# Performance work log

Measured on AMD Instinct MI355X. Metric: run time of the kernel, lower is better.

## Reference

```python
import jax, jax.numpy as jnp
import numpy as np

N_NODES = 50000
N_EDGES = 800000
D_IN = 128
D_OUT = 128
NEG_SLOPE = 0.2


def setup_inputs() -> dict:
    key = jax.random.key(0)
    ks = jax.random.split(key, 6)
    stdv = 1.0 / np.sqrt(D_OUT)
    X = jax.random.normal(ks[0], (N_NODES, D_IN), dtype=jnp.float32)
    W = jax.random.uniform(ks[1], (D_IN, D_OUT), dtype=jnp.float32, minval=-stdv, maxval=stdv)
    W_r = jax.random.uniform(ks[2], (D_IN, D_OUT), dtype=jnp.float32, minval=-stdv, maxval=stdv)
    W_l = jax.random.uniform(ks[3], (D_IN, D_OUT), dtype=jnp.float32, minval=-stdv, maxval=stdv)
    src = jax.random.randint(ks[4], (N_EDGES,), 0, N_NODES, dtype=jnp.int32)
    dst = jax.random.randint(ks[5], (N_EDGES,), 0, N_NODES, dtype=jnp.int32)
    return {"X": X, "W": W, "W_r": W_r, "W_l": W_l, "src": src, "dst": dst}


def reference(X, W, W_r, W_l, src, dst):
    # Dense transforms (comb/agg feature paths)
    comb = X @ W            # [N, D_out]
    h_r = X @ W_r           # [N, D_out]
    h_l = X @ W_l           # [N, D_out]
    # SDDMM: per-edge score e_ij = dot(h_l[i], h_r[j]) at nonzeros of A
    e = jnp.sum(h_l[src] * h_r[dst], axis=-1)          # [E]
    e = jax.nn.leaky_relu(e, negative_slope=NEG_SLOPE)  # LeakyReLU(0.2) on edge values
    # SpMM aggregation: agg[i] = sum_{j in N(i)} e_ij * comb[j]
    msgs = e[:, None] * comb[dst]                       # [E, D_out]
    agg = jax.ops.segment_sum(msgs, src, num_segments=N_NODES)  # [N, D_out]
    return agg
```

## Files before the change

### kernel.cpp

```cpp
#include <hip/hip_runtime.h>
#include <hip/hip_bf16.h>

#define N_NODES 50000
#define N_EDGES 800000
#define D 128
#define NEG_SLOPE 0.2f
#define APAD 136

#define FB 196
#define BCAP 8192
#define CHUNK 4096
#define BIN_NBLK ((N_EDGES + CHUNK - 1) / CHUNK)
#define CONV_NBLK (N_NODES * D / 4 / 256)
#define GEMM_LDS ((D + 64) * APAD * 2)

typedef __attribute__((ext_vector_type(8))) short bf16x8;
typedef __attribute__((ext_vector_type(4))) float f32x4;

__device__ inline unsigned short f2bf(float f) {
    union { float f; unsigned u; } v; v.f = f;
    const unsigned r = v.u + 0x7FFF + ((v.u >> 16) & 1);
    return (unsigned short)(r >> 16);
}
__device__ inline unsigned fbits(float f) { union { float f; unsigned u; } v; v.f = f; return v.u; }
__device__ inline float ffrom(unsigned u) { union { unsigned u; float f; } v; v.u = u; return v.f; }

__device__ inline void unpack8(const float4 raw, float* o) {
    const unsigned w0 = fbits(raw.x), w1 = fbits(raw.y), w2 = fbits(raw.z), w3 = fbits(raw.w);
    o[0] = ffrom(w0 << 16); o[1] = ffrom(w0 & 0xffff0000u);
    o[2] = ffrom(w1 << 16); o[3] = ffrom(w1 & 0xffff0000u);
    o[4] = ffrom(w2 << 16); o[5] = ffrom(w2 & 0xffff0000u);
    o[6] = ffrom(w3 << 16); o[7] = ffrom(w3 & 0xffff0000u);
}

__device__ inline int scan256_incl(int* arr, int t, int v) {
    arr[t] = v; __syncthreads();
#pragma unroll
    for (int off = 1; off < 256; off <<= 1) {
        const int u = (t >= off) ? arr[t - off] : 0;
        __syncthreads();
        arr[t] += u;
        __syncthreads();
    }
    return arr[t];
}

__global__ __launch_bounds__(256) void convert_prep_kernel(const float4* __restrict__ X,
                                                           ushort4* __restrict__ Xb,
                                                           const float* __restrict__ W_l,
                                                           const float* __restrict__ W_r,
                                                           const float* __restrict__ W,
                                                           ushort* __restrict__ MbT,
                                                           ushort* __restrict__ WbT,
                                                           int* __restrict__ bucket_fill) {
    if (blockIdx.x < CONV_NBLK) {
        const int i = blockIdx.x * 256 + threadIdx.x;
        const float4 v = X[i];
        ushort4 o;
        o.x = f2bf(v.x); o.y = f2bf(v.y); o.z = f2bf(v.z); o.w = f2bf(v.w);
        Xb[i] = o;
    } else {
        if (blockIdx.x == CONV_NBLK) bucket_fill[threadIdx.x] = 0;
        const int a = (blockIdx.x - CONV_NBLK) * 2 + (threadIdx.x >> 7);
        const int b2 = threadIdx.x & 127;
        float acc = 0.f;
#pragma unroll
        for (int c = 0; c < D; c += 4) {
            const float4 wl = *(const float4*)(W_l + a * D + c);
            const float4 wr = *(const float4*)(W_r + b2 * D + c);
            acc += wl.x * wr.x + wl.y * wr.y + wl.z * wr.z + wl.w * wr.w;
        }
        MbT[b2 * D + a] = f2bf(acc);
        WbT[b2 * D + a] = f2bf(W[a * D + b2]);
    }
}

__global__ __launch_bounds__(256) void bin_kernel(const int* __restrict__ src,
                                                  const int* __restrict__ dst,
                                                  int* __restrict__ bucket_fill,
                                                  int2* __restrict__ binned) {
    __shared__ int hist[256];
    __shared__ int bstart[256];
    __shared__ int reserveS[256];
    __shared__ int fillL[256];
    __shared__ int2 pairs[CHUNK];
    __shared__ int targ[CHUNK];
    const int t = threadIdx.x;
    const int e0 = blockIdx.x * CHUNK;

    hist[t] = 0;
    __syncthreads();

    int s[16], d[16], b[16];
#pragma unroll
    for (int i = 0; i < 16; ++i) {
        const int e = e0 + i * 256 + t;
        if (e < N_EDGES) {
            s[i] = src[e]; d[i] = dst[e]; b[i] = s[i] >> 8;
            atomicAdd(&hist[b[i]], 1);
        } else b[i] = -1;
    }
    __syncthreads();
    const int hv = hist[t];
    const int incl = scan256_incl(bstart, t, hv);
    const int mystart = incl - hv;
    reserveS[t] = hv ? atomicAdd(&bucket_fill[t], hv) : 0;
    __syncthreads();
    bstart[t] = mystart;
    fillL[t] = mystart;
    __syncthreads();
#pragma unroll
    for (int i = 0; i < 16; ++i) {
        if (b[i] >= 0) {
            const int p = atomicAdd(&fillL[b[i]], 1);
            pairs[p] = make_int2(s[i], d[i]);
            const int pos = reserveS[b[i]] + (p - bstart[b[i]]);
            targ[p] = (pos < BCAP) ? (b[i] * BCAP + pos) : -1;
        }
    }
    __syncthreads();
    const int nval = min(CHUNK, N_EDGES - e0);
    for (int j = t; j < nval; j += 256)
        if (targ[j] >= 0) binned[targ[j]] = pairs[j];
}

template <bool OUT_F32>
__device__ __forceinline__ void gemm_body(char* smemraw, int blk,
                                          const ushort* __restrict__ A,
                                          const ushort* __restrict__ BT,
                                          float* __restrict__ Cf,
                                          ushort* __restrict__ Cb,
                                          int nrows) {
    unsigned short* Bs = (unsigned short*)smemraw;
    unsigned short* As = Bs + D * APAD;
    const int tid = threadIdx.x;
    const int rb = blk * 64;

#pragma unroll
    for (int i = 0; i < 8; ++i) {
        const int idx = tid + i * 256;
        const int row = idx >> 4;
        const int c8 = (idx & 15) << 3;
        const float4 v = ((const float4*)BT)[idx];
        *(float4*)&Bs[row * APAD + c8] = v;
    }
#pragma unroll
    for (int i = 0; i < 4; ++i) {
        const int idx = tid + i * 256;
        const int row = idx >> 4;
        const int c8 = (idx & 15) << 3;
        float4 v = {0.f, 0.f, 0.f, 0.f};
        if (rb + row < nrows)
            v = ((const float4*)(A + (size_t)(rb + row) * D))[idx & 15];
        *(float4*)&As[row * APAD + c8] = v;
    }
    __syncthreads();

    const int w = tid >> 6;
    const int lane = tid & 63;
    const int m = lane & 15;
    const int kq = lane >> 4;

    f32x4 acc[8] = {};
    const unsigned short* Arow = &As[(w * 16 + m) * APAD + kq * 8];
#pragma unroll
    for (int kc = 0; kc < 4; ++kc) {
        const bf16x8 af = *(const bf16x8*)(Arow + kc * 32);
#pragma unroll
        for (int t2 = 0; t2 < 8; ++t2) {
            const bf16x8 bf = *(const bf16x8*)&Bs[(t2 * 16 + m) * APAD + kc * 32 + kq * 8];
            acc[t2] = __builtin_amdgcn_mfma_f32_16x16x32_bf16(af, bf, acc[t2], 0, 0, 0);
        }
    }

    const int orow0 = rb + w * 16 + kq * 4;
#pragma unroll
    for (int t2 = 0; t2 < 8; ++t2) {
#pragma unroll
        for (int r = 0; r < 4; ++r) {
            const int row = orow0 + r;
            if (row < nrows) {
                const size_t o = (size_t)row * D + t2 * 16 + m;
                if (OUT_F32) Cf[o] = acc[t2][r];
                else         Cb[o] = f2bf(acc[t2][r]);
            }
        }
    }
}

__global__ __launch_bounds__(256) void fine_gemm1_kernel(const int2* __restrict__ binned,
                                                         const int* __restrict__ bucket_fill,
                                                         int* __restrict__ offsets,
                                                         int* __restrict__ sorted_dst,
                                                         const ushort* __restrict__ Xb,
                                                         const ushort* __restrict__ MbT,
                                                         ushort* __restrict__ hMb) {
    __shared__ __align__(16) char smem[GEMM_LDS];
    if (blockIdx.x >= FB) {
        gemm_body<false>(smem, blockIdx.x - FB, Xb, MbT, nullptr, hMb, N_NODES);
        return;
    }
    int* cntS   = (int*)smem;
    int* nh     = cntS + 256;
    int* ex     = nh + 256;
    int* fill   = ex + 256;
    int* dstbuf = fill + 256;

    const int b = blockIdx.x;
    const int t = threadIdx.x;

    const int myc = (t < FB) ? bucket_fill[t] : 0;
    scan256_incl(cntS, t, myc);
    const int base = (b == 0) ? 0 : cntS[b - 1];
    int cnt = cntS[b] - base;
    if (cnt > BCAP) cnt = BCAP;

    nh[t] = 0;
    __syncthreads();
    const int2* bb = binned + (size_t)b * BCAP;
    for (int e = t; e < cnt; e += 256) atomicAdd(&nh[bb[e].x & 255], 1);
    __syncthreads();
    const int v = nh[t];
    const int incl2 = scan256_incl(ex, t, v);
    const int mystart = incl2 - v;
    const int node = b * 256 + t;
    if (node < N_NODES) offsets[node] = base + mystart;
    fill[t] = mystart;
    __syncthreads();
    for (int e = t; e < cnt; e += 256) {
        const int2 sd = bb[e];
        const int p = atomicAdd(&fill[sd.x & 255], 1);
        dstbuf[p] = sd.y;
    }
    __syncthreads();
    for (int j = t; j < cnt; j += 256)
        sorted_dst[base + j] = dstbuf[j];
}

__global__ __launch_bounds__(256) void gemm2_kernel(const ushort* __restrict__ A,
                                                    const ushort* __restrict__ BT,
                                                    float* __restrict__ Cf) {
    __shared__ __align__(16) char smem[GEMM_LDS];
    gemm_body<true>(smem, blockIdx.x, A, BT, Cf, nullptr, N_NODES);
}

__global__ __launch_bounds__(256) void spmm_kernel(const ushort* __restrict__ hMb,
                                                   const ushort* __restrict__ Xb,
                                                   const int* __restrict__ offsets,
                                                   const int* __restrict__ sorted_dst,
                                                   ushort* __restrict__ aggXb) {
    const int wave = threadIdx.x >> 6;
    const int lane = threadIdx.x & 63;
    const int node = blockIdx.x * 4 + wave;
    const int q = lane >> 4;
    const int ql = lane & 15;

    float hm[8];
    unpack8(*(const float4*)(hMb + (size_t)node * D + ql * 8), hm);

    const int start = offsets[node];
    const int end = (node == N_NODES - 1) ? N_EDGES : offsets[node + 1];

    float acc[8] = {0.f, 0.f, 0.f, 0.f, 0.f, 0.f, 0.f, 0.f};

    int idx = start + q;
    while (idx + 12 < end) {
        const int d0 = sorted_dst[idx];
        const int d1 = sorted_dst[idx + 4];
        const int d2 = sorted_dst[idx + 8];
        const int d3 = sorted_dst[idx + 12];
        const float4 r0 = *(const float4*)(Xb + (size_t)d0 * D + ql * 8);
        const float4 r1 = *(const float4*)(Xb + (size_t)d1 * D + ql * 8);
        const float4 r2 = *(const float4*)(Xb + (size_t)d2 * D + ql * 8);
        const float4 r3 = *(const float4*)(Xb + (size_t)d3 * D + ql * 8);
        float t0 = 0.f, t1 = 0.f, t2 = 0.f, t3 = 0.f;
        {
            float x[8];
            unpack8(r0, x);
#pragma unroll
            for (int j = 0; j < 8; ++j) t0 = fmaf(hm[j], x[j], t0);
            unpack8(r1, x);
#pragma unroll
            for (int j = 0; j < 8; ++j) t1 = fmaf(hm[j], x[j], t1);
            unpack8(r2, x);
#pragma unroll
            for (int j = 0; j < 8; ++j) t2 = fmaf(hm[j], x[j], t2);
            unpack8(r3, x);
#pragma unroll
            for (int j = 0; j < 8; ++j) t3 = fmaf(hm[j], x[j], t3);
        }
#pragma unroll
        for (int mm = 1; mm < 16; mm <<= 1) {
            t0 += __shfl_xor(t0, mm);
            t1 += __shfl_xor(t1, mm);
            t2 += __shfl_xor(t2, mm);
            t3 += __shfl_xor(t3, mm);
        }
        const float e0 = t0 > 0.f ? t0 : NEG_SLOPE * t0;
        const float e1 = t1 > 0.f ? t1 : NEG_SLOPE * t1;
        const float e2 = t2 > 0.f ? t2 : NEG_SLOPE * t2;
        const float e3 = t3 > 0.f ? t3 : NEG_SLOPE * t3;
        {
            float x[8];
            unpack8(r0, x);
#pragma unroll
            for (int j = 0; j < 8; ++j) acc[j] = fmaf(e0, x[j], acc[j]);
            unpack8(r1, x);
#pragma unroll
            for (int j = 0; j < 8; ++j) acc[j] = fmaf(e1, x[j], acc[j]);
            unpack8(r2, x);
#pragma unroll
            for (int j = 0; j < 8; ++j) acc[j] = fmaf(e2, x[j], acc[j]);
            unpack8(r3, x);
#pragma unroll
            for (int j = 0; j < 8; ++j) acc[j] = fmaf(e3, x[j], acc[j]);
        }
        idx += 16;
    }
    while (idx < end) {
        const int d0 = sorted_dst[idx];
        const float4 r0 = *(const float4*)(Xb + (size_t)d0 * D + ql * 8);
        float x[8];
        unpack8(r0, x);
        float t0 = 0.f;
#pragma unroll
        for (int j = 0; j < 8; ++j) t0 = fmaf(hm[j], x[j], t0);
#pragma unroll
        for (int mm = 1; mm < 16; mm <<= 1) t0 += __shfl_xor(t0, mm);
        const float e0 = t0 > 0.f ? t0 : NEG_SLOPE * t0;
#pragma unroll
        for (int j = 0; j < 8; ++j) acc[j] = fmaf(e0, x[j], acc[j]);
        idx += 4;
    }

#pragma unroll
    for (int j = 0; j < 8; ++j) {
        acc[j] += __shfl_xor(acc[j], 16);
        acc[j] += __shfl_xor(acc[j], 32);
    }
    if (q == 0) {
        ushort4 o0, o1;
        o0.x = f2bf(acc[0]); o0.y = f2bf(acc[1]); o0.z = f2bf(acc[2]); o0.w = f2bf(acc[3]);
        o1.x = f2bf(acc[4]); o1.y = f2bf(acc[5]); o1.z = f2bf(acc[6]); o1.w = f2bf(acc[7]);
        ushort* outp = aggXb + (size_t)node * D + ql * 8;
        *(ushort4*)outp = o0;
        *(ushort4*)(outp + 4) = o1;
    }
}

extern "C" void kernel_launch(void* const* d_in, const int* in_sizes, int n_in,
                              void* d_out, int out_size, void* d_ws, size_t ws_size,
                              hipStream_t stream) {
    const float* X   = (const float*)d_in[0];
    const float* W   = (const float*)d_in[1];
    const float* W_r = (const float*)d_in[2];
    const float* W_l = (const float*)d_in[3];
    const int* src   = (const int*)d_in[4];
    const int* dst   = (const int*)d_in[5];
    float* agg = (float*)d_out;

    ushort* Xb          = (ushort*)d_ws;
    ushort* hMb         = Xb + (size_t)N_NODES * D;
    ushort* aggXb       = hMb + (size_t)N_NODES * D;
    ushort* MbT         = aggXb + (size_t)N_NODES * D;
    ushort* WbT         = MbT + D * D;
    int*    offsets     = (int*)(WbT + D * D);
    int*    sorted_dst  = offsets + N_NODES;
    int*    bucket_fill = sorted_dst + N_EDGES;
    int2*   binned      = (int2*)(bucket_fill + 256);

    convert_prep_kernel<<<CONV_NBLK + 64, 256, 0, stream>>>(
        (const float4*)X, (ushort4*)Xb, W_l, W_r, W, MbT, WbT, bucket_fill);

    bin_kernel<<<BIN_NBLK, 256, 0, stream>>>(src, dst, bucket_fill, binned);

    fine_gemm1_kernel<<<FB + (N_NODES + 63) / 64, 256, 0, stream>>>(
        binned, bucket_fill, offsets, sorted_dst, Xb, MbT, hMb);

    spmm_kernel<<<N_NODES / 4, 256, 0, stream>>>(hMb, Xb, offsets, sorted_dst, aggXb);

    gemm2_kernel<<<(N_NODES + 63) / 64, 256, 0, stream>>>(aggXb, WbT, agg);
}
```

Before: 179.5 us.

## Fuse X conversion into GEMM1 and SpMM into GEMM2, regroup kernel stages

Moves the fp32-to-bf16 conversion of X into the first GEMM kernel, so the converted tile goes straight to LDS and is also written out for the SpMM. Fuses the SpMM aggregation with the final GEMM: each block aggregates 64 nodes into an LDS tile and multiplies by W, which removes the aggXb round trip through global memory. It also merges binning with the weight prep, replaces the in-kernel counter reset with a memset, and splits fine sorting into its own kernel, which loses the overlap fine sorting previously had with GEMM1. In the SpMM, each 16-lane group now walks one node at a time, processing 4 nodes in sequence instead of splitting one node's edges across 4 groups, so there is less parallelism per node and more risk of load imbalance.

```diff
diff --git a/kernel.cpp b/kernel.cpp
--- a/kernel.cpp
+++ b/kernel.cpp
@@ -11,8 +11,8 @@
 #define BCAP 8192
 #define CHUNK 4096
 #define BIN_NBLK ((N_EDGES + CHUNK - 1) / CHUNK)
-#define CONV_NBLK (N_NODES * D / 4 / 256)
-#define GEMM_LDS ((D + 64) * APAD * 2)
+#define GROWS 64
+#define GGRID ((N_NODES + GROWS - 1) / GROWS)
 
 typedef __attribute__((ext_vector_type(8))) short bf16x8;
 typedef __attribute__((ext_vector_type(4))) float f32x4;
@@ -45,97 +45,8 @@
     return arr[t];
 }
 
-__global__ __launch_bounds__(256) void convert_prep_kernel(const float4* __restrict__ X,
-                                                           ushort4* __restrict__ Xb,
-                                                           const float* __restrict__ W_l,
-                                                           const float* __restrict__ W_r,
-                                                           const float* __restrict__ W,
-                                                           ushort* __restrict__ MbT,
-                                                           ushort* __restrict__ WbT,
-                                                           int* __restrict__ bucket_fill) {
-    if (blockIdx.x < CONV_NBLK) {
-        const int i = blockIdx.x * 256 + threadIdx.x;
-        const float4 v = X[i];
-        ushort4 o;
-        o.x = f2bf(v.x); o.y = f2bf(v.y); o.z = f2bf(v.z); o.w = f2bf(v.w);
-        Xb[i] = o;
-    } else {
-        if (blockIdx.x == CONV_NBLK) bucket_fill[threadIdx.x] = 0;
-        const int a = (blockIdx.x - CONV_NBLK) * 2 + (threadIdx.x >> 7);
-        const int b2 = threadIdx.x & 127;
-        float acc = 0.f;
-#pragma unroll
-        for (int c = 0; c < D; c += 4) {
-            const float4 wl = *(const float4*)(W_l + a * D + c);
-            const float4 wr = *(const float4*)(W_r + b2 * D + c);
-            acc += wl.x * wr.x + wl.y * wr.y + wl.z * wr.z + wl.w * wr.w;
-        }
-        MbT[b2 * D + a] = f2bf(acc);
-        WbT[b2 * D + a] = f2bf(W[a * D + b2]);
-    }
-}
-
-__global__ __launch_bounds__(256) void bin_kernel(const int* __restrict__ src,
-                                                  const int* __restrict__ dst,
-                                                  int* __restrict__ bucket_fill,
-                                                  int2* __restrict__ binned) {
-    __shared__ int hist[256];
-    __shared__ int bstart[256];
-    __shared__ int reserveS[256];
-    __shared__ int fillL[256];
-    __shared__ int2 pairs[CHUNK];
-    __shared__ int targ[CHUNK];
-    const int t = threadIdx.x;
-    const int e0 = blockIdx.x * CHUNK;
-
-    hist[t] = 0;
-    __syncthreads();
-
-    int s[16], d[16], b[16];
-#pragma unroll
-    for (int i = 0; i < 16; ++i) {
-        const int e = e0 + i * 256 + t;
-        if (e < N_EDGES) {
-            s[i] = src[e]; d[i] = dst[e]; b[i] = s[i] >> 8;
-            atomicAdd(&hist[b[i]], 1);
-        } else b[i] = -1;
-    }
-    __syncthreads();
-    const int hv = hist[t];
-    const int incl = scan256_incl(bstart, t, hv);
-    const int mystart = incl - hv;
-    reserveS[t] = hv ? atomicAdd(&bucket_fill[t], hv) : 0;
-    __syncthreads();
-    bstart[t] = mystart;
-    fillL[t] = mystart;
-    __syncthreads();
-#pragma unroll
-    for (int i = 0; i < 16; ++i) {
-        if (b[i] >= 0) {
-            const int p = atomicAdd(&fillL[b[i]], 1);
-            pairs[p] = make_int2(s[i], d[i]);
-            const int pos = reserveS[b[i]] + (p - bstart[b[i]]);
-            targ[p] = (pos < BCAP) ? (b[i] * BCAP + pos) : -1;
-        }
-    }
-    __syncthreads();
-    const int nval = min(CHUNK, N_EDGES - e0);
-    for (int j = t; j < nval; j += 256)
-        if (targ[j] >= 0) binned[targ[j]] = pairs[j];
-}
-
-template <bool OUT_F32>
-__device__ __forceinline__ void gemm_body(char* smemraw, int blk,
-                                          const ushort* __restrict__ A,
-                                          const ushort* __restrict__ BT,
-                                          float* __restrict__ Cf,
-                                          ushort* __restrict__ Cb,
-                                          int nrows) {
-    unsigned short* Bs = (unsigned short*)smemraw;
-    unsigned short* As = Bs + D * APAD;
+__device__ __forceinline__ void stage_B_lds(unsigned short* Bs, const ushort* __restrict__ BT) {
     const int tid = threadIdx.x;
-    const int rb = blk * 64;
-
 #pragma unroll
     for (int i = 0; i < 8; ++i) {
         const int idx = tid + i * 256;
@@ -144,23 +55,15 @@
         const float4 v = ((const float4*)BT)[idx];
         *(float4*)&Bs[row * APAD + c8] = v;
     }
-#pragma unroll
-    for (int i = 0; i < 4; ++i) {
-        const int idx = tid + i * 256;
-        const int row = idx >> 4;
-        const int c8 = (idx & 15) << 3;
-        float4 v = {0.f, 0.f, 0.f, 0.f};
-        if (rb + row < nrows)
-            v = ((const float4*)(A + (size_t)(rb + row) * D))[idx & 15];
-        *(float4*)&As[row * APAD + c8] = v;
-    }
-    __syncthreads();
-
-    const int w = tid >> 6;
-    const int lane = tid & 63;
-    const int m = lane & 15;
-    const int kq = lane >> 4;
-
+}
+
+template <bool OUT_F32>
+__device__ __forceinline__ void mfma_from_lds(const unsigned short* Bs,
+                                              const unsigned short* As,
+                                              int rb, float* __restrict__ Cf,
+                                              ushort* __restrict__ Cb, int nrows) {
+    const int tid = threadIdx.x;
+    const int w = tid >> 6, lane = tid & 63, m = lane & 15, kq = lane >> 4;
     f32x4 acc[8] = {};
     const unsigned short* Arow = &As[(w * 16 + m) * APAD + kq * 8];
 #pragma unroll
@@ -172,7 +75,6 @@
             acc[t2] = __builtin_amdgcn_mfma_f32_16x16x32_bf16(af, bf, acc[t2], 0, 0, 0);
         }
     }
-
     const int orow0 = rb + w * 16 + kq * 4;
 #pragma unroll
     for (int t2 = 0; t2 < 8; ++t2) {
@@ -188,24 +90,116 @@
     }
 }
 
-__global__ __launch_bounds__(256) void fine_gemm1_kernel(const int2* __restrict__ binned,
-                                                         const int* __restrict__ bucket_fill,
-                                                         int* __restrict__ offsets,
-                                                         int* __restrict__ sorted_dst,
-                                                         const ushort* __restrict__ Xb,
-                                                         const ushort* __restrict__ MbT,
-                                                         ushort* __restrict__ hMb) {
-    __shared__ __align__(16) char smem[GEMM_LDS];
-    if (blockIdx.x >= FB) {
-        gemm_body<false>(smem, blockIdx.x - FB, Xb, MbT, nullptr, hMb, N_NODES);
-        return;
-    }
-    int* cntS   = (int*)smem;
-    int* nh     = cntS + 256;
-    int* ex     = nh + 256;
-    int* fill   = ex + 256;
-    int* dstbuf = fill + 256;
-
+__global__ __launch_bounds__(256) void bin_prep_kernel(const int* __restrict__ src,
+                                                       const int* __restrict__ dst,
+                                                       int* __restrict__ bucket_fill,
+                                                       int2* __restrict__ binned,
+                                                       const float* __restrict__ W_l,
+                                                       const float* __restrict__ W_r,
+                                                       const float* __restrict__ W,
+                                                       ushort* __restrict__ MbT,
+                                                       ushort* __restrict__ WbT) {
+    if (blockIdx.x < BIN_NBLK) {
+        __shared__ int hist[256];
+        __shared__ int bstart[256];
+        __shared__ int reserveS[256];
+        __shared__ int fillL[256];
+        __shared__ int2 pairs[CHUNK];
+        __shared__ int targ[CHUNK];
+        const int t = threadIdx.x;
+        const int e0 = blockIdx.x * CHUNK;
+
+        hist[t] = 0;
+        __syncthreads();
+
+        int s[16], d[16], b[16];
+#pragma unroll
+        for (int i = 0; i < 16; ++i) {
+            const int e = e0 + i * 256 + t;
+            if (e < N_EDGES) {
+                s[i] = src[e]; d[i] = dst[e]; b[i] = s[i] >> 8;
+                atomicAdd(&hist[b[i]], 1);
+            } else b[i] = -1;
+        }
+        __syncthreads();
+        const int hv = hist[t];
+        const int incl = scan256_incl(bstart, t, hv);
+        const int mystart = incl - hv;
+        reserveS[t] = hv ? atomicAdd(&bucket_fill[t], hv) : 0;
+        __syncthreads();
+        bstart[t] = mystart;
+        fillL[t] = mystart;
+        __syncthreads();
+#pragma unroll
+        for (int i = 0; i < 16; ++i) {
+            if (b[i] >= 0) {
+                const int p = atomicAdd(&fillL[b[i]], 1);
+                pairs[p] = make_int2(s[i], d[i]);
+                const int pos = reserveS[b[i]] + (p - bstart[b[i]]);
+                targ[p] = (pos < BCAP) ? (b[i] * BCAP + pos) : -1;
+            }
+        }
+        __syncthreads();
+        const int nval = min(CHUNK, N_EDGES - e0);
+        for (int j = t; j < nval; j += 256)
+            if (targ[j] >= 0) binned[targ[j]] = pairs[j];
+    } else {
+        const int a = (blockIdx.x - BIN_NBLK) * 2 + (threadIdx.x >> 7);
+        const int b2 = threadIdx.x & 127;
+        float acc = 0.f;
+#pragma unroll
+        for (int c = 0; c < D; c += 4) {
+            const float4 wl = *(const float4*)(W_l + a * D + c);
+            const float4 wr = *(const float4*)(W_r + b2 * D + c);
+            acc += wl.x * wr.x + wl.y * wr.y + wl.z * wr.z + wl.w * wr.w;
+        }
+        MbT[b2 * D + a] = f2bf(acc);
+        WbT[b2 * D + a] = f2bf(W[a * D + b2]);
+    }
+}
+
+__global__ __launch_bounds__(256) void convert_gemm1_kernel(const float4* __restrict__ Xf4,
+                                                            ushort* __restrict__ Xb,
+                                                            const ushort* __restrict__ MbT,
+                                                            ushort* __restrict__ hMb) {
+    __shared__ __align__(16) unsigned short Bs[D * APAD];
+    __shared__ __align__(16) unsigned short As[GROWS * APAD];
+    const int t = threadIdx.x;
+    const int rb = blockIdx.x * GROWS;
+
+    stage_B_lds(Bs, MbT);
+
+#pragma unroll
+    for (int i = 0; i < 4; ++i) {
+        const int f2 = t + i * 256;
+        const int row = f2 >> 4;
+        const int c8 = (f2 & 15) << 3;
+        ushort4 lo = {0, 0, 0, 0}, hi = {0, 0, 0, 0};
+        if (rb + row < N_NODES) {
+            const float4 a = Xf4[(size_t)(rb + row) * 32 + (c8 >> 2)];
+            const float4 b = Xf4[(size_t)(rb + row) * 32 + (c8 >> 2) + 1];
+            lo.x = f2bf(a.x); lo.y = f2bf(a.y); lo.z = f2bf(a.z); lo.w = f2bf(a.w);
+            hi.x = f2bf(b.x); hi.y = f2bf(b.y); hi.z = f2bf(b.z); hi.w = f2bf(b.w);
+            ushort* gp = Xb + (size_t)(rb + row) * D + c8;
+            *(ushort4*)gp = lo;
+            *(ushort4*)(gp + 4) = hi;
+        }
+        *(ushort4*)&As[row * APAD + c8] = lo;
+        *(ushort4*)&As[row * APAD + c8 + 4] = hi;
+    }
+    __syncthreads();
+    mfma_from_lds<false>(Bs, As, rb, nullptr, hMb, N_NODES);
+}
+
+__global__ __launch_bounds__(256) void fine_kernel(const int2* __restrict__ binned,
+                                                   const int* __restrict__ bucket_fill,
+                                                   int* __restrict__ offsets,
+                                                   int* __restrict__ sorted_dst) {
+    __shared__ int cntS[256];
+    __shared__ int nh[256];
+    __shared__ int ex[256];
+    __shared__ int fill[256];
+    __shared__ int dstbuf[BCAP];
     const int b = blockIdx.x;
     const int t = threadIdx.x;
 
@@ -237,115 +231,109 @@
         sorted_dst[base + j] = dstbuf[j];
 }
 
-__global__ __launch_bounds__(256) void gemm2_kernel(const ushort* __restrict__ A,
-                                                    const ushort* __restrict__ BT,
-                                                    float* __restrict__ Cf) {
-    __shared__ __align__(16) char smem[GEMM_LDS];
-    gemm_body<true>(smem, blockIdx.x, A, BT, Cf, nullptr, N_NODES);
-}
-
-__global__ __launch_bounds__(256) void spmm_kernel(const ushort* __restrict__ hMb,
-                                                   const ushort* __restrict__ Xb,
-                                                   const int* __restrict__ offsets,
-                                                   const int* __restrict__ sorted_dst,
-                                                   ushort* __restrict__ aggXb) {
-    const int wave = threadIdx.x >> 6;
-    const int lane = threadIdx.x & 63;
-    const int node = blockIdx.x * 4 + wave;
-    const int q = lane >> 4;
-    const int ql = lane & 15;
-
-    float hm[8];
-    unpack8(*(const float4*)(hMb + (size_t)node * D + ql * 8), hm);
-
-    const int start = offsets[node];
-    const int end = (node == N_NODES - 1) ? N_EDGES : offsets[node + 1];
-
-    float acc[8] = {0.f, 0.f, 0.f, 0.f, 0.f, 0.f, 0.f, 0.f};
-
-    int idx = start + q;
-    while (idx + 12 < end) {
-        const int d0 = sorted_dst[idx];
-        const int d1 = sorted_dst[idx + 4];
-        const int d2 = sorted_dst[idx + 8];
-        const int d3 = sorted_dst[idx + 12];
-        const float4 r0 = *(const float4*)(Xb + (size_t)d0 * D + ql * 8);
-        const float4 r1 = *(const float4*)(Xb + (size_t)d1 * D + ql * 8);
-        const float4 r2 = *(const float4*)(Xb + (size_t)d2 * D + ql * 8);
-        const float4 r3 = *(const float4*)(Xb + (size_t)d3 * D + ql * 8);
-        float t0 = 0.f, t1 = 0.f, t2 = 0.f, t3 = 0.f;
-        {
-            float x[8];
-            unpack8(r0, x);
-#pragma unroll
-            for (int j = 0; j < 8; ++j) t0 = fmaf(hm[j], x[j], t0);
-            unpack8(r1, x);
-#pragma unroll
-            for (int j = 0; j < 8; ++j) t1 = fmaf(hm[j], x[j], t1);
-            unpack8(r2, x);
-#pragma unroll
-            for (int j = 0; j < 8; ++j) t2 = fmaf(hm[j], x[j], t2);
-            unpack8(r3, x);
-#pragma unroll
-            for (int j = 0; j < 8; ++j) t3 = fmaf(hm[j], x[j], t3);
-        }
-#pragma unroll
-        for (int mm = 1; mm < 16; mm <<= 1) {
-            t0 += __shfl_xor(t0, mm);
-            t1 += __shfl_xor(t1, mm);
-            t2 += __shfl_xor(t2, mm);
-            t3 += __shfl_xor(t3, mm);
-        }
-        const float e0 = t0 > 0.f ? t0 : NEG_SLOPE * t0;
-        const float e1 = t1 > 0.f ? t1 : NEG_SLOPE * t1;
-        const float e2 = t2 > 0.f ? t2 : NEG_SLOPE * t2;
-        const float e3 = t3 > 0.f ? t3 : NEG_SLOPE * t3;
-        {
-            float x[8];
-            unpack8(r0, x);
-#pragma unroll
-            for (int j = 0; j < 8; ++j) acc[j] = fmaf(e0, x[j], acc[j]);
-            unpack8(r1, x);
-#pragma unroll
-            for (int j = 0; j < 8; ++j) acc[j] = fmaf(e1, x[j], acc[j]);
-            unpack8(r2, x);
-#pragma unroll
-            for (int j = 0; j < 8; ++j) acc[j] = fmaf(e2, x[j], acc[j]);
-            unpack8(r3, x);
-#pragma unroll
-            for (int j = 0; j < 8; ++j) acc[j] = fmaf(e3, x[j], acc[j]);
-        }
-        idx += 16;
-    }
-    while (idx < end) {
-        const int d0 = sorted_dst[idx];
-        const float4 r0 = *(const float4*)(Xb + (size_t)d0 * D + ql * 8);
-        float x[8];
-        unpack8(r0, x);
-        float t0 = 0.f;
-#pragma unroll
-        for (int j = 0; j < 8; ++j) t0 = fmaf(hm[j], x[j], t0);
-#pragma unroll
-        for (int mm = 1; mm < 16; mm <<= 1) t0 += __shfl_xor(t0, mm);
-        const float e0 = t0 > 0.f ? t0 : NEG_SLOPE * t0;
-#pragma unroll
-        for (int j = 0; j < 8; ++j) acc[j] = fmaf(e0, x[j], acc[j]);
-        idx += 4;
-    }
-
-#pragma unroll
-    for (int j = 0; j < 8; ++j) {
-        acc[j] += __shfl_xor(acc[j], 16);
-        acc[j] += __shfl_xor(acc[j], 32);
-    }
-    if (q == 0) {
+__global__ __launch_bounds__(256) void spmm_gemm2_kernel(const ushort* __restrict__ hMb,
+                                                         const ushort* __restrict__ Xb,
+                                                         const int* __restrict__ offsets,
+                                                         const int* __restrict__ sorted_dst,
+                                                         const ushort* __restrict__ WbT,
+                                                         float* __restrict__ agg) {
+    __shared__ __align__(16) unsigned short Bs[D * APAD];
+    __shared__ __align__(16) unsigned short aggl[GROWS * APAD];
+    const int t = threadIdx.x;
+    const int rb = blockIdx.x * GROWS;
+    const int lane = t & 63, w = t >> 6;
+    const int q = lane >> 4, ql = lane & 15;
+    const int qid = w * 4 + q;
+
+    stage_B_lds(Bs, WbT);
+
+    for (int i = 0; i < 4; ++i) {
+        const int node = rb + qid * 4 + i;
+        float acc[8] = {0.f, 0.f, 0.f, 0.f, 0.f, 0.f, 0.f, 0.f};
+        if (node < N_NODES) {
+            float hm[8];
+            unpack8(*(const float4*)(hMb + (size_t)node * D + ql * 8), hm);
+            const int start = offsets[node];
+            const int end = (node == N_NODES - 1) ? N_EDGES : offsets[node + 1];
+            int idx = start;
+            while (idx + 3 < end) {
+                const int d0 = sorted_dst[idx];
+                const int d1 = sorted_dst[idx + 1];
+                const int d2 = sorted_dst[idx + 2];
+                const int d3 = sorted_dst[idx + 3];
+                const float4 r0 = *(const float4*)(Xb + (size_t)d0 * D + ql * 8);
+                const float4 r1 = *(const float4*)(Xb + (size_t)d1 * D + ql * 8);
+                const float4 r2 = *(const float4*)(Xb + (size_t)d2 * D + ql * 8);
+                const float4 r3 = *(const float4*)(Xb + (size_t)d3 * D + ql * 8);
+                float t0 = 0.f, t1 = 0.f, t2 = 0.f, t3 = 0.f;
+                {
+                    float x[8];
+                    unpack8(r0, x);
+#pragma unroll
+                    for (int j = 0; j < 8; ++j) t0 = fmaf(hm[j], x[j], t0);
+                    unpack8(r1, x);
+#pragma unroll
+                    for (int j = 0; j < 8; ++j) t1 = fmaf(hm[j], x[j], t1);
+                    unpack8(r2, x);
+#pragma unroll
+                    for (int j = 0; j < 8; ++j) t2 = fmaf(hm[j], x[j], t2);
+                    unpack8(r3, x);
+#pragma unroll
+                    for (int j = 0; j < 8; ++j) t3 = fmaf(hm[j], x[j], t3);
+                }
+#pragma unroll
+                for (int mm = 1; mm < 16; mm <<= 1) {
+                    t0 += __shfl_xor(t0, mm);
+                    t1 += __shfl_xor(t1, mm);
+                    t2 += __shfl_xor(t2, mm);
+                    t3 += __shfl_xor(t3, mm);
+                }
+                const float e0 = t0 > 0.f ? t0 : NEG_SLOPE * t0;
+                const float e1 = t1 > 0.f ? t1 : NEG_SLOPE * t1;
+                const float e2 = t2 > 0.f ? t2 : NEG_SLOPE * t2;
+                const float e3 = t3 > 0.f ? t3 : NEG_SLOPE * t3;
+                {
+                    float x[8];
+                    unpack8(r0, x);
+#pragma unroll
+                    for (int j = 0; j < 8; ++j) acc[j] = fmaf(e0, x[j], acc[j]);
+                    unpack8(r1, x);
+#pragma unroll
+                    for (int j = 0; j < 8; ++j) acc[j] = fmaf(e1, x[j], acc[j]);
+                    unpack8(r2, x);
+#pragma unroll
+                    for (int j = 0; j < 8; ++j) acc[j] = fmaf(e2, x[j], acc[j]);
+                    unpack8(r3, x);
+#pragma unroll
+                    for (int j = 0; j < 8; ++j) acc[j] = fmaf(e3, x[j], acc[j]);
+                }
+                idx += 4;
+            }
+            while (idx < end) {
+                const int d0 = sorted_dst[idx];
+                const float4 r0 = *(const float4*)(Xb + (size_t)d0 * D + ql * 8);
+                float x[8];
+                unpack8(r0, x);
+                float t0 = 0.f;
+#pragma unroll
+                for (int j = 0; j < 8; ++j) t0 = fmaf(hm[j], x[j], t0);
+#pragma unroll
+                for (int mm = 1; mm < 16; mm <<= 1) t0 += __shfl_xor(t0, mm);
+                const float e0 = t0 > 0.f ? t0 : NEG_SLOPE * t0;
+#pragma unroll
+                for (int j = 0; j < 8; ++j) acc[j] = fmaf(e0, x[j], acc[j]);
+                ++idx;
+            }
+        }
         ushort4 o0, o1;
         o0.x = f2bf(acc[0]); o0.y = f2bf(acc[1]); o0.z = f2bf(acc[2]); o0.w = f2bf(acc[3]);
         o1.x = f2bf(acc[4]); o1.y = f2bf(acc[5]); o1.z = f2bf(acc[6]); o1.w = f2bf(acc[7]);
-        ushort* outp = aggXb + (size_t)node * D + ql * 8;
-        *(ushort4*)outp = o0;
-        *(ushort4*)(outp + 4) = o1;
-    }
+        unsigned short* lp = &aggl[(qid * 4 + i) * APAD + ql * 8];
+        *(ushort4*)lp = o0;
+        *(ushort4*)(lp + 4) = o1;
+    }
+    __syncthreads();
+    mfma_from_lds<true>(Bs, aggl, rb, agg, nullptr, N_NODES);
 }
 
 extern "C" void kernel_launch(void* const* d_in, const int* in_sizes, int n_in,
@@ -361,23 +349,23 @@
 
     ushort* Xb          = (ushort*)d_ws;
     ushort* hMb         = Xb + (size_t)N_NODES * D;
-    ushort* aggXb       = hMb + (size_t)N_NODES * D;
-    ushort* MbT         = aggXb + (size_t)N_NODES * D;
+    ushort* MbT         = hMb + (size_t)N_NODES * D;
     ushort* WbT         = MbT + D * D;
     int*    offsets     = (int*)(WbT + D * D);
     int*    sorted_dst  = offsets + N_NODES;
     int*    bucket_fill = sorted_dst + N_EDGES;
     int2*   binned      = (int2*)(bucket_fill + 256);
 
-    convert_prep_kernel<<<CONV_NBLK + 64, 256, 0, stream>>>(
-        (const float4*)X, (ushort4*)Xb, W_l, W_r, W, MbT, WbT, bucket_fill);
-
-    bin_kernel<<<BIN_NBLK, 256, 0, stream>>>(src, dst, bucket_fill, binned);
-
-    fine_gemm1_kernel<<<FB + (N_NODES + 63) / 64, 256, 0, stream>>>(
-        binned, bucket_fill, offsets, sorted_dst, Xb, MbT, hMb);
-
-    spmm_kernel<<<N_NODES / 4, 256, 0, stream>>>(hMb, Xb, offsets, sorted_dst, aggXb);
-
-    gemm2_kernel<<<(N_NODES + 63) / 64, 256, 0, stream>>>(aggXb, WbT, agg);
-}
+    hipMemsetAsync(bucket_fill, 0, 256 * sizeof(int), stream);
+
+    bin_prep_kernel<<<BIN_NBLK + 64, 256, 0, stream>>>(
+        src, dst, bucket_fill, binned, W_l, W_r, W, MbT, WbT);
+
+    fine_kernel<<<FB, 256, 0, stream>>>(binned, bucket_fill, offsets, sorted_dst);
+
+    convert_gemm1_kernel<<<GGRID, 256, 0, stream>>>(
+        (const float4*)X, Xb, MbT, hMb);
+
+    spmm_gemm2_kernel<<<GGRID, 256, 0, stream>>>(
+        hMb, Xb, offsets, sorted_dst, WbT, agg);
+}
```

Measured after the change: 185.7 us. 3.5% more time.
